# Kernel tuning notes

Measured on AMD Instinct MI355X. Metric: run time of the kernel, lower is better.

Reference implementation:

```python
import jax, jax.numpy as jnp
import numpy as np

N = 50000
T = 6
E = 800000
F_IN = 64
HID = 64
HEADS = 4
NEG_SLOPE = 0.2
BN_EPS = 1e-5


def _gat_layer(x, src, dst, W, att_src, att_dst, bias, concat):
    # x: [N, Fin]; W: [Fin, H*C]; att_*: [H, C]; src/dst: [E+N] (self loops appended)
    n = x.shape[0]
    H, C = att_src.shape
    xl = (x @ W).reshape(n, H, C)                     # [N, H, C]
    a_src = jnp.sum(xl * att_src[None], axis=-1)      # [N, H]
    a_dst = jnp.sum(xl * att_dst[None], axis=-1)      # [N, H]
    e = jax.nn.leaky_relu(a_src[src] + a_dst[dst], NEG_SLOPE)  # [E', H]
    # segment softmax over destination nodes (every node has a self loop)
    m = jax.ops.segment_max(e, dst, num_segments=n)
    ex = jnp.exp(e - m[dst])
    s = jax.ops.segment_sum(ex, dst, num_segments=n)
    alpha = ex / (s[dst] + 1e-16)                     # [E', H]
    msg = alpha[:, :, None] * xl[src]                 # [E', H, C]
    out = jax.ops.segment_sum(msg, dst, num_segments=n)  # [N, H, C]
    if concat:
        out = out.reshape(n, H * C)
    else:
        out = out.mean(axis=1)
    return out + bias


def _forward(x_seq, edge_index, W1, as1, ad1, b1, W2, as2, ad2, b2,
             cw1, cb1, g1, be1, cw2, cb2, g2, be2, lw1, lb1, lw2, lb2):
    n = x_seq.shape[1]
    self_loop = jnp.arange(n, dtype=edge_index.dtype)
    src = jnp.concatenate([edge_index[0], self_loop])
    dst = jnp.concatenate([edge_index[1], self_loop])

    def per_t(x):
        h = _gat_layer(x, src, dst, W1, as1, ad1, b1, concat=True)
        h = jax.nn.elu(h)
        h = _gat_layer(h, src, dst, W2, as2, ad2, b2, concat=False)
        h = jax.nn.elu(h)
        return h                                      # [N, HID]

    temporal = jax.vmap(per_t)(x_seq)                 # [T, N, HID]
    temporal = jnp.transpose(temporal, (1, 2, 0))     # [N, HID, T]

    def conv_bn_relu(t, cw, cb, g, be):
        y = jax.lax.conv_general_dilated(
            t, cw, window_strides=(1,), padding=[(1, 1)],
            dimension_numbers=('NCH', 'OIH', 'NCH')) + cb[None, :, None]
        # BatchNorm1d in eval mode, running_mean=0, running_var=1
        y = y * (g / jnp.sqrt(1.0 + BN_EPS))[None, :, None] + be[None, :, None]
        return jax.nn.relu(y)

    t = conv_bn_relu(temporal, cw1, cb1, g1, be1)
    t = conv_bn_relu(t, cw2, cb2, g2, be2)
    pooled = t.mean(axis=-1)                          # adaptive avg pool -> [N, HID]
    h = jax.nn.relu(pooled @ lw1 + lb1)
    logits = h @ lw2 + lb2                            # [N, 1]
    return logits


def setup_inputs() -> dict:
    key = jax.random.key(0)
    ks = jax.random.split(key, 20)
    C1 = HID // HEADS  # 16
    s = 0.1
    return {
        'x_seq': jax.random.normal(ks[0], (T, N, F_IN), jnp.float32),
        'edge_index': jax.random.randint(ks[1], (2, E), 0, N, jnp.int32),
        'W1': jax.random.normal(ks[2], (F_IN, HEADS * C1), jnp.float32) * s,
        'as1': jax.random.normal(ks[3], (HEADS, C1), jnp.float32) * s,
        'ad1': jax.random.normal(ks[4], (HEADS, C1), jnp.float32) * s,
        'b1': jnp.zeros((HEADS * C1,), jnp.float32),
        'W2': jax.random.normal(ks[5], (HID, HEADS * HID), jnp.float32) * s,
        'as2': jax.random.normal(ks[6], (HEADS, HID), jnp.float32) * s,
        'ad2': jax.random.normal(ks[7], (HEADS, HID), jnp.float32) * s,
        'b2': jnp.zeros((HID,), jnp.float32),
        'cw1': jax.random.normal(ks[8], (HID, HID, 3), jnp.float32) * s,
        'cb1': jnp.zeros((HID,), jnp.float32),
        'g1': jnp.ones((HID,), jnp.float32),
        'be1': jnp.zeros((HID,), jnp.float32),
        'cw2': jax.random.normal(ks[9], (HID, HID, 3), jnp.float32) * s,
        'cb2': jnp.zeros((HID,), jnp.float32),
        'g2': jnp.ones((HID,), jnp.float32),
        'be2': jnp.zeros((HID,), jnp.float32),
        'lw1': jax.random.normal(ks[10], (HID, HID // 2), jnp.float32) * s,
        'lb1': jnp.zeros((HID // 2,), jnp.float32),
        'lw2': jax.random.normal(ks[11], (HID // 2, 1), jnp.float32) * s,
        'lb2': jnp.zeros((1,), jnp.float32),
    }


def reference(x_seq, edge_index, W1, as1, ad1, b1, W2, as2, ad2, b2,
              cw1, cb1, g1, be1, cw2, cb2, g2, be2, lw1, lb1, lw2, lb2):
    return _forward(x_seq, edge_index, W1, as1, ad1, b1, W2, as2, ad2, b2,
                    cw1, cb1, g1, be1, cw2, cb2, g2, be2, lw1, lb1, lw2, lb2)
```

## Files before the change

kernel.cpp:

```cpp
#include <hip/hip_runtime.h>
#include <math.h>

#define NN 50000
#define EE 800000
#define TT 6

__device__ __forceinline__ float lrelu(float x){ return x > 0.f ? x : 0.2f*x; }
__device__ __forceinline__ float eluf(float x){ return x > 0.f ? x : expm1f(x); }

__global__ void k_init_counts(int* __restrict__ c){
  int i = blockIdx.x*256 + threadIdx.x;
  if (i < NN) c[i] = 1;
}

__global__ void k_hist(const int* __restrict__ dst, int* __restrict__ c){
  int i = blockIdx.x*256 + threadIdx.x;
  if (i < EE) atomicAdd(&c[dst[i]], 1);
}

__global__ void k_scanA(const int* __restrict__ cnt, int* __restrict__ excl,
                        int* __restrict__ bsum){
  __shared__ int sh[1024];
  int tid = threadIdx.x;
  int i = blockIdx.x*1024 + tid;
  int v = (i < NN) ? cnt[i] : 0;
  int x = v;
  sh[tid] = x; __syncthreads();
  for (int off = 1; off < 1024; off <<= 1){
    int y = (tid >= off) ? sh[tid - off] : 0;
    __syncthreads();
    x += y; sh[tid] = x; __syncthreads();
  }
  if (i < NN) excl[i] = x - v;
  if (tid == 1023) bsum[blockIdx.x] = x;
}

__global__ void k_scanB(int* __restrict__ bsum, int nb){
  if (threadIdx.x == 0){
    int run = 0;
    for (int b = 0; b < nb; ++b){ int t = bsum[b]; bsum[b] = run; run += t; }
  }
}

__global__ void k_scanC(const int* __restrict__ excl, const int* __restrict__ bsum,
                        int* __restrict__ rowptr, int* __restrict__ cursor){
  int i = blockIdx.x*1024 + threadIdx.x;
  if (i < NN){
    int v = excl[i] + bsum[blockIdx.x];
    rowptr[i] = v; cursor[i] = v;
  }
  if (i == 0) rowptr[NN] = EE + NN;
}

__global__ void k_scatter(const int* __restrict__ ei, int* __restrict__ cursor,
                          int* __restrict__ csr){
  int i = blockIdx.x*256 + threadIdx.x;
  if (i < EE){
    int d = ei[EE + i];
    int p = atomicAdd(&cursor[d], 1);
    csr[p] = ei[i];
  } else if (i < EE + NN){
    int v = i - EE;
    int p = atomicAdd(&cursor[v], 1);
    csr[p] = v;
  }
}

__global__ void k_prep(const float* __restrict__ W1, const float* __restrict__ as1,
                       const float* __restrict__ ad1,
                       const float* __restrict__ W2, const float* __restrict__ as2,
                       const float* __restrict__ ad2,
                       const float* __restrict__ cw1, const float* __restrict__ cw2,
                       const float* __restrict__ lw1,
                       float* __restrict__ Was1, float* __restrict__ Wad1,
                       float* __restrict__ Wat2, float* __restrict__ Wb,
                       float4* __restrict__ wq1, float4* __restrict__ wq2,
                       float* __restrict__ lw1t){
  int tid = threadIdx.x;
  int k = tid >> 2, h = tid & 3;
  float s1 = 0.f, d1 = 0.f, s2 = 0.f, d2 = 0.f;
  for (int c = 0; c < 16; ++c){
    float w = W1[k*64 + h*16 + c];
    s1 += w * as1[h*16 + c];
    d1 += w * ad1[h*16 + c];
  }
  for (int c = 0; c < 64; ++c){
    float w = W2[k*256 + h*64 + c];
    s2 += w * as2[h*64 + c];
    d2 += w * ad2[h*64 + c];
  }
  Was1[k*4+h] = s1; Wad1[k*4+h] = d1;
  Wat2[k*8 + h] = s2; Wat2[k*8 + 4 + h] = d2;
  for (int idx = tid; idx < 256*64; idx += 256){
    int kf = idx >> 6, c = idx & 63;
    int hh = kf >> 6, kk = kf & 63;
    Wb[idx] = W2[kk*256 + hh*64 + c];
  }
  for (int idx = tid; idx < 64*64; idx += 256){
    int o = idx >> 6, i = idx & 63;
    wq1[idx] = make_float4(cw1[o*192+i*3], cw1[o*192+i*3+1], cw1[o*192+i*3+2], 0.f);
    wq2[idx] = make_float4(cw2[o*192+i*3], cw2[o*192+i*3+1], cw2[o*192+i*3+2], 0.f);
  }
  for (int idx = tid; idx < 32*64; idx += 256){
    int j = idx >> 6, kk = idx & 63;
    lw1t[idx] = lw1[kk*32 + j];
  }
}

__global__ __launch_bounds__(256) void k_gemm_att1(const float* __restrict__ A,
                            const float* __restrict__ W,
                            const float* __restrict__ Was, const float* __restrict__ Wad,
                            float* __restrict__ Xl, float* __restrict__ a_src,
                            float* __restrict__ a_dst){
  __shared__ float At[64][16];
  int tid = threadIdx.x;
  int r0 = blockIdx.x * 16;
  {
    const float4* A4 = (const float4*)(A + (size_t)r0*64);
    float4 v = A4[tid];
    int r = tid >> 4, k4 = (tid & 15) << 2;
    At[k4+0][r] = v.x; At[k4+1][r] = v.y;
    At[k4+2][r] = v.z; At[k4+3][r] = v.w;
  }
  __syncthreads();
  int col = tid & 63;
  int rbase = (tid >> 6) << 2;
  float acc0=0.f, acc1=0.f, acc2=0.f, acc3=0.f;
  for (int k = 0; k < 64; ++k){
    float w = W[k*64 + col];
    float4 a4 = *(const float4*)&At[k][rbase];
    acc0 += a4.x*w; acc1 += a4.y*w; acc2 += a4.z*w; acc3 += a4.w*w;
  }
  Xl[(size_t)(r0+rbase+0)*64 + col] = acc0;
  Xl[(size_t)(r0+rbase+1)*64 + col] = acc1;
  Xl[(size_t)(r0+rbase+2)*64 + col] = acc2;
  Xl[(size_t)(r0+rbase+3)*64 + col] = acc3;
  if (tid < 128){
    int r = tid >> 3, jx = tid & 7;
    int h = jx & 3;
    const float* Wv = (jx < 4) ? Was : Wad;
    float a = 0.f;
    for (int k = 0; k < 64; ++k) a += At[k][r] * Wv[k*4 + h];
    if (jx < 4) a_src[(r0 + r)*4 + h] = a;
    else        a_dst[(r0 + r)*4 + h] = a;
  }
}

__global__ __launch_bounds__(256) void k_agg1(
                       const float* __restrict__ xl, const float* __restrict__ a_src,
                       const float* __restrict__ a_dst, const float* __restrict__ b1,
                       const float* __restrict__ Wat2,
                       const int* __restrict__ rowptr, const int* __restrict__ csr,
                       float* __restrict__ h1,
                       float* __restrict__ a_src2, float* __restrict__ a_dst2){
  int lane = threadIdx.x & 63;
  int wid  = threadIdx.x >> 6;
  int n = blockIdx.x*4 + wid;
  int h = lane >> 4;
  float ad = a_dst[n*4 + h];
  int rs = rowptr[n], re = rowptr[n+1];
  float s = 0.f, acc = 0.f;
  int j = rs;
  for (; j + 8 <= re; j += 8){
    int sn0=csr[j],   sn1=csr[j+1], sn2=csr[j+2], sn3=csr[j+3];
    int sn4=csr[j+4], sn5=csr[j+5], sn6=csr[j+6], sn7=csr[j+7];
    float e0=a_src[sn0*4+h], e1=a_src[sn1*4+h], e2=a_src[sn2*4+h], e3=a_src[sn3*4+h];
    float e4=a_src[sn4*4+h], e5=a_src[sn5*4+h], e6=a_src[sn6*4+h], e7=a_src[sn7*4+h];
    float x0=xl[(size_t)sn0*64+lane], x1=xl[(size_t)sn1*64+lane];
    float x2=xl[(size_t)sn2*64+lane], x3=xl[(size_t)sn3*64+lane];
    float x4=xl[(size_t)sn4*64+lane], x5=xl[(size_t)sn5*64+lane];
    float x6=xl[(size_t)sn6*64+lane], x7=xl[(size_t)sn7*64+lane];
    float p0=__expf(lrelu(e0+ad)), p1=__expf(lrelu(e1+ad));
    float p2=__expf(lrelu(e2+ad)), p3=__expf(lrelu(e3+ad));
    float p4=__expf(lrelu(e4+ad)), p5=__expf(lrelu(e5+ad));
    float p6=__expf(lrelu(e6+ad)), p7=__expf(lrelu(e7+ad));
    s += p0; acc += p0*x0;
    s += p1; acc += p1*x1;
    s += p2; acc += p2*x2;
    s += p3; acc += p3*x3;
    s += p4; acc += p4*x4;
    s += p5; acc += p5*x5;
    s += p6; acc += p6*x6;
    s += p7; acc += p7*x7;
  }
  for (; j < re; ++j){
    int sn = csr[j];
    float p = __expf(lrelu(a_src[sn*4+h] + ad));
    float x = xl[(size_t)sn*64 + lane];
    s += p; acc += p*x;
  }
  float hv = eluf(acc/(s + 1e-16f) + b1[lane]);
  h1[(size_t)n*64 + lane] = hv;
  float4 wA = ((const float4*)Wat2)[lane*2];
  float4 wB = ((const float4*)Wat2)[lane*2 + 1];
  float p[8];
  p[0]=hv*wA.x; p[1]=hv*wA.y; p[2]=hv*wA.z; p[3]=hv*wA.w;
  p[4]=hv*wB.x; p[5]=hv*wB.y; p[6]=hv*wB.z; p[7]=hv*wB.w;
#pragma unroll
  for (int off = 32; off >= 1; off >>= 1){
#pragma unroll
    for (int q = 0; q < 8; ++q) p[q] += __shfl_xor(p[q], off);
  }
  if (lane == 0){
    ((float4*)a_src2)[n] = make_float4(p[0],p[1],p[2],p[3]);
    ((float4*)a_dst2)[n] = make_float4(p[4],p[5],p[6],p[7]);
  }
}

__global__ __launch_bounds__(256) void k_agg2(
                       const float* __restrict__ h1, const float* __restrict__ a_src,
                       const float* __restrict__ a_dst,
                       const int* __restrict__ rowptr, const int* __restrict__ csr,
                       float* __restrict__ agg){
  int lane = threadIdx.x & 63;
  int wid  = threadIdx.x >> 6;
  int n = blockIdx.x*4 + wid;
  float4 ad = ((const float4*)a_dst)[n];
  int rs = rowptr[n], re = rowptr[n+1];
  float s0=0.f,s1=0.f,s2=0.f,s3=0.f;
  float g0=0.f,g1=0.f,g2=0.f,g3=0.f;
  int j = rs;
  for (; j + 8 <= re; j += 8){
    int sa=csr[j],   sb=csr[j+1], sc=csr[j+2], sd=csr[j+3];
    int se=csr[j+4], sf=csr[j+5], sg=csr[j+6], sh=csr[j+7];
    float4 ea = ((const float4*)a_src)[sa];
    float4 eb = ((const float4*)a_src)[sb];
    float4 ec = ((const float4*)a_src)[sc];
    float4 ed = ((const float4*)a_src)[sd];
    float4 ee = ((const float4*)a_src)[se];
    float4 ef = ((const float4*)a_src)[sf];
    float4 eg = ((const float4*)a_src)[sg];
    float4 eh = ((const float4*)a_src)[sh];
    float xa = h1[(size_t)sa*64 + lane];
    float xb = h1[(size_t)sb*64 + lane];
    float xc = h1[(size_t)sc*64 + lane];
    float xd = h1[(size_t)sd*64 + lane];
    float xe = h1[(size_t)se*64 + lane];
    float xf = h1[(size_t)sf*64 + lane];
    float xg = h1[(size_t)sg*64 + lane];
    float xh = h1[(size_t)sh*64 + lane];
    float pa0=__expf(lrelu(ea.x+ad.x)), pa1=__expf(lrelu(ea.y+ad.y));
    float pa2=__expf(lrelu(ea.z+ad.z)), pa3=__expf(lrelu(ea.w+ad.w));
    float pb0=__expf(lrelu(eb.x+ad.x)), pb1=__expf(lrelu(eb.y+ad.y));
    float pb2=__expf(lrelu(eb.z+ad.z)), pb3=__expf(lrelu(eb.w+ad.w));
    float pc0=__expf(lrelu(ec.x+ad.x)), pc1=__expf(lrelu(ec.y+ad.y));
    float pc2=__expf(lrelu(ec.z+ad.z)), pc3=__expf(lrelu(ec.w+ad.w));
    float pd0=__expf(lrelu(ed.x+ad.x)), pd1=__expf(lrelu(ed.y+ad.y));
    float pd2=__expf(lrelu(ed.z+ad.z)), pd3=__expf(lrelu(ed.w+ad.w));
    float pe0=__expf(lrelu(ee.x+ad.x)), pe1=__expf(lrelu(ee.y+ad.y));
    float pe2=__expf(lrelu(ee.z+ad.z)), pe3=__expf(lrelu(ee.w+ad.w));
    float pf0=__expf(lrelu(ef.x+ad.x)), pf1=__expf(lrelu(ef.y+ad.y));
    float pf2=__expf(lrelu(ef.z+ad.z)), pf3=__expf(lrelu(ef.w+ad.w));
    float pg0=__expf(lrelu(eg.x+ad.x)), pg1=__expf(lrelu(eg.y+ad.y));
    float pg2=__expf(lrelu(eg.z+ad.z)), pg3=__expf(lrelu(eg.w+ad.w));
    float ph0=__expf(lrelu(eh.x+ad.x)), ph1=__expf(lrelu(eh.y+ad.y));
    float ph2=__expf(lrelu(eh.z+ad.z)), ph3=__expf(lrelu(eh.w+ad.w));
    s0 += pa0+pb0+pc0+pd0+pe0+pf0+pg0+ph0;
    g0 += pa0*xa + pb0*xb + pc0*xc + pd0*xd + pe0*xe + pf0*xf + pg0*xg + ph0*xh;
    s1 += pa1+pb1+pc1+pd1+pe1+pf1+pg1+ph1;
    g1 += pa1*xa + pb1*xb + pc1*xc + pd1*xd + pe1*xe + pf1*xf + pg1*xg + ph1*xh;
    s2 += pa2+pb2+pc2+pd2+pe2+pf2+pg2+ph2;
    g2 += pa2*xa + pb2*xb + pc2*xc + pd2*xd + pe2*xe + pf2*xf + pg2*xg + ph2*xh;
    s3 += pa3+pb3+pc3+pd3+pe3+pf3+pg3+ph3;
    g3 += pa3*xa + pb3*xb + pc3*xc + pd3*xd + pe3*xe + pf3*xf + pg3*xg + ph3*xh;
  }
  for (; j < re; ++j){
    int sn = csr[j];
    float4 ev = ((const float4*)a_src)[sn];
    float x = h1[(size_t)sn*64 + lane];
    float p0=__expf(lrelu(ev.x+ad.x)), p1=__expf(lrelu(ev.y+ad.y));
    float p2=__expf(lrelu(ev.z+ad.z)), p3=__expf(lrelu(ev.w+ad.w));
    s0 += p0; g0 += p0*x;
    s1 += p1; g1 += p1*x;
    s2 += p2; g2 += p2*x;
    s3 += p3; g3 += p3*x;
  }
  size_t base = (size_t)n*256 + lane;
  agg[base      ] = g0/(s0 + 1e-16f);
  agg[base +  64] = g1/(s1 + 1e-16f);
  agg[base + 128] = g2/(s2 + 1e-16f);
  agg[base + 192] = g3/(s3 + 1e-16f);
}

__global__ __launch_bounds__(256) void k_out2(const float* __restrict__ agg,
                                              const float* __restrict__ Wb,
                                              const float* __restrict__ b2,
                                              float* __restrict__ ht){
  __shared__ float AtF[256*20];
  int tid = threadIdx.x;
  int r0 = blockIdx.x * 16;
  const float4* A4 = (const float4*)(agg + (size_t)r0*256);
#pragma unroll
  for (int jj = 0; jj < 4; ++jj){
    int m = tid + 256*jj;
    float4 v = A4[m];
    int row = m >> 6, k0 = (m & 63) << 2;
    AtF[(k0+0)*20 + row] = v.x;
    AtF[(k0+1)*20 + row] = v.y;
    AtF[(k0+2)*20 + row] = v.z;
    AtF[(k0+3)*20 + row] = v.w;
  }
  __syncthreads();
  int col = tid & 63;
  int rbase = (tid >> 6) << 2;
  float acc0=0.f, acc1=0.f, acc2=0.f, acc3=0.f;
  for (int k = 0; k < 256; ++k){
    float w = Wb[(size_t)k*64 + col];
    float4 a4 = *(const float4*)&AtF[k*20 + rbase];
    acc0 += a4.x*w; acc1 += a4.y*w; acc2 += a4.z*w; acc3 += a4.w*w;
  }
  float bb = b2[col];
  ht[(size_t)(r0+rbase+0)*64 + col] = eluf(0.25f*acc0 + bb);
  ht[(size_t)(r0+rbase+1)*64 + col] = eluf(0.25f*acc1 + bb);
  ht[(size_t)(r0+rbase+2)*64 + col] = eluf(0.25f*acc2 + bb);
  ht[(size_t)(r0+rbase+3)*64 + col] = eluf(0.25f*acc3 + bb);
}

__global__ __launch_bounds__(256) void k_conv(const float* __restrict__ htb,
    const float4* __restrict__ wq1, const float* __restrict__ cb1,
    const float* __restrict__ g1,   const float* __restrict__ be1,
    const float4* __restrict__ wq2, const float* __restrict__ cb2,
    const float* __restrict__ g2,   const float* __restrict__ be2,
    float* __restrict__ pooledG){
  __shared__ float X[64*198];
  int tid  = threadIdx.x;
  int lane = tid & 63;
  int w    = __builtin_amdgcn_readfirstlane(tid >> 6);
  int nn   = lane & 31;
  int half = lane >> 5;
  int n0 = blockIdx.x*32;
  int n  = n0 + nn;
  int ob = w*16 + half*8;

#pragma unroll
  for (int k = 0; k < 8; ++k){
    int p  = k*256 + tid;
    int ch = p & 63, ns = p >> 6;
    int nsrc = n0 + ns; if (nsrc >= NN) nsrc = NN-1;
    float xv[6];
#pragma unroll
    for (int t = 0; t < 6; ++t) xv[t] = htb[((size_t)t*NN + nsrc)*64 + ch];
#pragma unroll
    for (int t = 0; t < 6; ++t) X[ch*198 + t*33 + ns] = xv[t];
  }
  __syncthreads();

  float acc[8][6];
#pragma unroll
  for (int o = 0; o < 8; ++o){
    float c = cb1[ob+o];
#pragma unroll
    for (int t = 0; t < 6; ++t) acc[o][t] = c;
  }
  for (int i = 0; i < 64; ++i){
    const float* xp = X + i*198 + nn;
    float x1 = xp[0], x2 = xp[33], x3 = xp[66];
    float x4 = xp[99], x5 = xp[132], x6 = xp[165];
#pragma unroll
    for (int o = 0; o < 8; ++o){
      float4 wv = wq1[(ob+o)*64 + i];
      acc[o][0] += wv.y*x1 + wv.z*x2;
      acc[o][1] += wv.x*x1 + wv.y*x2 + wv.z*x3;
      acc[o][2] += wv.x*x2 + wv.y*x3 + wv.z*x4;
      acc[o][3] += wv.x*x3 + wv.y*x4 + wv.z*x5;
      acc[o][4] += wv.x*x4 + wv.y*x5 + wv.z*x6;
      acc[o][5] += wv.x*x5 + wv.y*x6;
    }
  }
  __syncthreads();
#pragma unroll
  for (int o = 0; o < 8; ++o){
    float bns = g1[ob+o]*rsqrtf(1.f + 1e-5f), be = be1[ob+o];
    float* xp = X + (ob+o)*198 + nn;
#pragma unroll
    for (int t = 0; t < 6; ++t) xp[t*33] = fmaxf(acc[o][t]*bns + be, 0.f);
  }
  __syncthreads();

#pragma unroll
  for (int o = 0; o < 8; ++o){
    float c = cb2[ob+o];
#pragma unroll
    for (int t = 0; t < 6; ++t) acc[o][t] = c;
  }
  for (int i = 0; i < 64; ++i){
    const float* xp = X + i*198 + nn;
    float x1 = xp[0], x2 = xp[33], x3 = xp[66];
    float x4 = xp[99], x5 = xp[132], x6 = xp[165];
#pragma unroll
    for (int o = 0; o < 8; ++o){
      float4 wv = wq2[(ob+o)*64 + i];
      acc[o][0] += wv.y*x1 + wv.z*x2;
      acc[o][1] += wv.x*x1 + wv.y*x2 + wv.z*x3;
      acc[o][2] += wv.x*x2 + wv.y*x3 + wv.z*x4;
      acc[o][3] += wv.x*x3 + wv.y*x4 + wv.z*x5;
      acc[o][4] += wv.x*x4 + wv.y*x5 + wv.z*x6;
      acc[o][5] += wv.x*x5 + wv.y*x6;
    }
  }
  if (n < NN){
#pragma unroll
    for (int o = 0; o < 8; ++o){
      float bns = g2[ob+o]*rsqrtf(1.f + 1e-5f), be = be2[ob+o];
      float pooled = 0.f;
#pragma unroll
      for (int t = 0; t < 6; ++t) pooled += fmaxf(acc[o][t]*bns + be, 0.f);
      pooledG[(size_t)(ob+o)*NN + n] = pooled*(1.f/6.f);
    }
  }
}

__global__ __launch_bounds__(256) void k_mlp(const float* __restrict__ pooledG,
    const float* __restrict__ lw1t, const float* __restrict__ lb1,
    const float* __restrict__ lw2,  const float* __restrict__ lb2,
    float* __restrict__ out){
  int lane = threadIdx.x & 63;
  int w = __builtin_amdgcn_readfirstlane(threadIdx.x >> 6);
  int n = (blockIdx.x*4 + w)*64 + lane;
  int nc = (n < NN) ? n : (NN-1);
  float p[64];
#pragma unroll 16
  for (int o = 0; o < 64; ++o) p[o] = pooledG[(size_t)o*NN + nc];
  float po = 0.f;
  for (int j = 0; j < 32; ++j){
    float hj = lb1[j];
#pragma unroll 16
    for (int k = 0; k < 64; ++k) hj += p[k] * lw1t[j*64 + k];
    po += fmaxf(hj, 0.f) * lw2[j];
  }
  if (n < NN) out[n] = po + lb2[0];
}

extern "C" void kernel_launch(void* const* d_in, const int* in_sizes, int n_in,
                              void* d_out, int out_size, void* d_ws, size_t ws_size,
                              hipStream_t stream) {
  const float* x_seq = (const float*)d_in[0];
  const int*   ei    = (const int*)  d_in[1];
  const float* W1  = (const float*)d_in[2];
  const float* as1 = (const float*)d_in[3];
  const float* ad1 = (const float*)d_in[4];
  const float* b1  = (const float*)d_in[5];
  const float* W2  = (const float*)d_in[6];
  const float* as2 = (const float*)d_in[7];
  const float* ad2 = (const float*)d_in[8];
  const float* b2  = (const float*)d_in[9];
  const float* cw1 = (const float*)d_in[10];
  const float* cb1 = (const float*)d_in[11];
  const float* g1  = (const float*)d_in[12];
  const float* be1 = (const float*)d_in[13];
  const float* cw2 = (const float*)d_in[14];
  const float* cb2 = (const float*)d_in[15];
  const float* g2  = (const float*)d_in[16];
  const float* be2 = (const float*)d_in[17];
  const float* lw1 = (const float*)d_in[18];
  const float* lb1 = (const float*)d_in[19];
  const float* lw2 = (const float*)d_in[20];
  const float* lb2 = (const float*)d_in[21];
  float* out = (float*)d_out;

  char* wp = (char*)d_ws;
  auto alloc = [&](size_t bytes) -> char* {
    char* p = wp; wp += (bytes + 255) & ~(size_t)255; return p;
  };
  int*   counts = (int*)  alloc(NN*sizeof(int));
  int*   excl   = (int*)  alloc(NN*sizeof(int));
  int*   bsum   = (int*)  alloc(64*sizeof(int));
  int*   rowptr = (int*)  alloc((NN+1)*sizeof(int));
  int*   cursor = (int*)  alloc(NN*sizeof(int));
  int*   csr    = (int*)  alloc((size_t)(EE+NN)*sizeof(int));
  float* a_src1 = (float*)alloc((size_t)NN*4*sizeof(float));
  float* a_dst1 = (float*)alloc((size_t)NN*4*sizeof(float));
  float* a_src2 = (float*)alloc((size_t)NN*4*sizeof(float));
  float* a_dst2 = (float*)alloc((size_t)NN*4*sizeof(float));
  float* h1     = (float*)alloc((size_t)NN*64*sizeof(float));
  float* agg    = (float*)alloc((size_t)NN*256*sizeof(float));
  float* xl1    = agg;
  float* htb    = (float*)alloc((size_t)TT*NN*64*sizeof(float));
  float* pooledG= (float*)alloc((size_t)64*NN*sizeof(float));
  float* Was1 = (float*)alloc(256*sizeof(float));
  float* Wad1 = (float*)alloc(256*sizeof(float));
  float* Wat2 = (float*)alloc(64*8*sizeof(float));
  float* Wb   = (float*)alloc(256*64*sizeof(float));
  float4* wq1 = (float4*)alloc(64*64*sizeof(float4));
  float4* wq2 = (float4*)alloc(64*64*sizeof(float4));
  float* lw1t = (float*)alloc(32*64*sizeof(float));

  const int NBSCAN = (NN + 1023)/1024;
  k_init_counts<<<(NN+255)/256, 256, 0, stream>>>(counts);
  k_hist<<<(EE+255)/256, 256, 0, stream>>>(ei + EE, counts);
  k_scanA<<<NBSCAN, 1024, 0, stream>>>(counts, excl, bsum);
  k_scanB<<<1, 64, 0, stream>>>(bsum, NBSCAN);
  k_scanC<<<NBSCAN, 1024, 0, stream>>>(excl, bsum, rowptr, cursor);
  k_scatter<<<(EE+NN+255)/256, 256, 0, stream>>>(ei, cursor, csr);
  k_prep<<<1, 256, 0, stream>>>(W1, as1, ad1, W2, as2, ad2, cw1, cw2, lw1,
                                Was1, Wad1, Wat2, Wb, wq1, wq2, lw1t);

  for (int t = 0; t < TT; ++t){
    const float* xt = x_seq + (size_t)t*NN*64;
    k_gemm_att1<<<NN/16, 256, 0, stream>>>(xt, W1, Was1, Wad1, xl1, a_src1, a_dst1);
    k_agg1<<<NN/4, 256, 0, stream>>>(xl1, a_src1, a_dst1, b1, Wat2, rowptr, csr,
                                     h1, a_src2, a_dst2);
    k_agg2<<<NN/4, 256, 0, stream>>>(h1, a_src2, a_dst2, rowptr, csr, agg);
    k_out2<<<NN/16, 256, 0, stream>>>(agg, Wb, b2, htb + (size_t)t*NN*64);
  }
  k_conv<<<(NN+31)/32, 256, 0, stream>>>(htb, wq1, cb1, g1, be1, wq2, cb2, g2, be2,
                                         pooledG);
  k_mlp<<<(NN+255)/256, 256, 0, stream>>>(pooledG, lw1t, lb1, lw2, lb2, out);
}
```

Measured before the change: 1.554 ms.

## Retile out2 GEMM and conv kernel, shrink gather unroll in aggregation

The edge-gather loops in both aggregation kernels are unrolled by 4 instead of 8, which lowers register pressure and may raise occupancy at the cost of fewer loads in flight. The layer-2 output GEMM is re-tiled so each block stages 64 rows of agg in padded shared memory. Each lane owns one row and accumulates 16 output columns with wave-uniform weight reads, and results are written back through shared memory for coalesced stores. The temporal conv kernel now processes 16 nodes per block with 4 output channels per thread, giving smaller shared memory and register footprints and more blocks.

```diff
diff --git a/kernel.cpp b/kernel.cpp
--- a/kernel.cpp
+++ b/kernel.cpp
@@ -161,27 +161,17 @@
   int rs = rowptr[n], re = rowptr[n+1];
   float s = 0.f, acc = 0.f;
   int j = rs;
-  for (; j + 8 <= re; j += 8){
-    int sn0=csr[j],   sn1=csr[j+1], sn2=csr[j+2], sn3=csr[j+3];
-    int sn4=csr[j+4], sn5=csr[j+5], sn6=csr[j+6], sn7=csr[j+7];
+  for (; j + 4 <= re; j += 4){
+    int sn0=csr[j], sn1=csr[j+1], sn2=csr[j+2], sn3=csr[j+3];
     float e0=a_src[sn0*4+h], e1=a_src[sn1*4+h], e2=a_src[sn2*4+h], e3=a_src[sn3*4+h];
-    float e4=a_src[sn4*4+h], e5=a_src[sn5*4+h], e6=a_src[sn6*4+h], e7=a_src[sn7*4+h];
     float x0=xl[(size_t)sn0*64+lane], x1=xl[(size_t)sn1*64+lane];
     float x2=xl[(size_t)sn2*64+lane], x3=xl[(size_t)sn3*64+lane];
-    float x4=xl[(size_t)sn4*64+lane], x5=xl[(size_t)sn5*64+lane];
-    float x6=xl[(size_t)sn6*64+lane], x7=xl[(size_t)sn7*64+lane];
     float p0=__expf(lrelu(e0+ad)), p1=__expf(lrelu(e1+ad));
     float p2=__expf(lrelu(e2+ad)), p3=__expf(lrelu(e3+ad));
-    float p4=__expf(lrelu(e4+ad)), p5=__expf(lrelu(e5+ad));
-    float p6=__expf(lrelu(e6+ad)), p7=__expf(lrelu(e7+ad));
     s += p0; acc += p0*x0;
     s += p1; acc += p1*x1;
     s += p2; acc += p2*x2;
     s += p3; acc += p3*x3;
-    s += p4; acc += p4*x4;
-    s += p5; acc += p5*x5;
-    s += p6; acc += p6*x6;
-    s += p7; acc += p7*x7;
   }
   for (; j < re; ++j){
     int sn = csr[j];
@@ -220,25 +210,16 @@
   float s0=0.f,s1=0.f,s2=0.f,s3=0.f;
   float g0=0.f,g1=0.f,g2=0.f,g3=0.f;
   int j = rs;
-  for (; j + 8 <= re; j += 8){
-    int sa=csr[j],   sb=csr[j+1], sc=csr[j+2], sd=csr[j+3];
-    int se=csr[j+4], sf=csr[j+5], sg=csr[j+6], sh=csr[j+7];
+  for (; j + 4 <= re; j += 4){
+    int sa=csr[j], sb=csr[j+1], sc=csr[j+2], sd=csr[j+3];
     float4 ea = ((const float4*)a_src)[sa];
     float4 eb = ((const float4*)a_src)[sb];
     float4 ec = ((const float4*)a_src)[sc];
     float4 ed = ((const float4*)a_src)[sd];
-    float4 ee = ((const float4*)a_src)[se];
-    float4 ef = ((const float4*)a_src)[sf];
-    float4 eg = ((const float4*)a_src)[sg];
-    float4 eh = ((const float4*)a_src)[sh];
     float xa = h1[(size_t)sa*64 + lane];
     float xb = h1[(size_t)sb*64 + lane];
     float xc = h1[(size_t)sc*64 + lane];
     float xd = h1[(size_t)sd*64 + lane];
-    float xe = h1[(size_t)se*64 + lane];
-    float xf = h1[(size_t)sf*64 + lane];
-    float xg = h1[(size_t)sg*64 + lane];
-    float xh = h1[(size_t)sh*64 + lane];
     float pa0=__expf(lrelu(ea.x+ad.x)), pa1=__expf(lrelu(ea.y+ad.y));
     float pa2=__expf(lrelu(ea.z+ad.z)), pa3=__expf(lrelu(ea.w+ad.w));
     float pb0=__expf(lrelu(eb.x+ad.x)), pb1=__expf(lrelu(eb.y+ad.y));
@@ -247,22 +228,10 @@
     float pc2=__expf(lrelu(ec.z+ad.z)), pc3=__expf(lrelu(ec.w+ad.w));
     float pd0=__expf(lrelu(ed.x+ad.x)), pd1=__expf(lrelu(ed.y+ad.y));
     float pd2=__expf(lrelu(ed.z+ad.z)), pd3=__expf(lrelu(ed.w+ad.w));
-    float pe0=__expf(lrelu(ee.x+ad.x)), pe1=__expf(lrelu(ee.y+ad.y));
-    float pe2=__expf(lrelu(ee.z+ad.z)), pe3=__expf(lrelu(ee.w+ad.w));
-    float pf0=__expf(lrelu(ef.x+ad.x)), pf1=__expf(lrelu(ef.y+ad.y));
-    float pf2=__expf(lrelu(ef.z+ad.z)), pf3=__expf(lrelu(ef.w+ad.w));
-    float pg0=__expf(lrelu(eg.x+ad.x)), pg1=__expf(lrelu(eg.y+ad.y));
-    float pg2=__expf(lrelu(eg.z+ad.z)), pg3=__expf(lrelu(eg.w+ad.w));
-    float ph0=__expf(lrelu(eh.x+ad.x)), ph1=__expf(lrelu(eh.y+ad.y));
-    float ph2=__expf(lrelu(eh.z+ad.z)), ph3=__expf(lrelu(eh.w+ad.w));
-    s0 += pa0+pb0+pc0+pd0+pe0+pf0+pg0+ph0;
-    g0 += pa0*xa + pb0*xb + pc0*xc + pd0*xd + pe0*xe + pf0*xf + pg0*xg + ph0*xh;
-    s1 += pa1+pb1+pc1+pd1+pe1+pf1+pg1+ph1;
-    g1 += pa1*xa + pb1*xb + pc1*xc + pd1*xd + pe1*xe + pf1*xf + pg1*xg + ph1*xh;
-    s2 += pa2+pb2+pc2+pd2+pe2+pf2+pg2+ph2;
-    g2 += pa2*xa + pb2*xb + pc2*xc + pd2*xd + pe2*xe + pf2*xf + pg2*xg + ph2*xh;
-    s3 += pa3+pb3+pc3+pd3+pe3+pf3+pg3+ph3;
-    g3 += pa3*xa + pb3*xb + pc3*xc + pd3*xd + pe3*xe + pf3*xf + pg3*xg + ph3*xh;
+    s0 += pa0+pb0+pc0+pd0; g0 += pa0*xa + pb0*xb + pc0*xc + pd0*xd;
+    s1 += pa1+pb1+pc1+pd1; g1 += pa1*xa + pb1*xb + pc1*xc + pd1*xd;
+    s2 += pa2+pb2+pc2+pd2; g2 += pa2*xa + pb2*xb + pc2*xc + pd2*xd;
+    s3 += pa3+pb3+pc3+pd3; g3 += pa3*xa + pb3*xb + pc3*xc + pd3*xd;
   }
   for (; j < re; ++j){
     int sn = csr[j];
@@ -286,34 +255,42 @@
                                               const float* __restrict__ Wb,
                                               const float* __restrict__ b2,
                                               float* __restrict__ ht){
-  __shared__ float AtF[256*20];
+  __shared__ float A[64*257];
   int tid = threadIdx.x;
-  int r0 = blockIdx.x * 16;
-  const float4* A4 = (const float4*)(agg + (size_t)r0*256);
-#pragma unroll
-  for (int jj = 0; jj < 4; ++jj){
-    int m = tid + 256*jj;
-    float4 v = A4[m];
-    int row = m >> 6, k0 = (m & 63) << 2;
-    AtF[(k0+0)*20 + row] = v.x;
-    AtF[(k0+1)*20 + row] = v.y;
-    AtF[(k0+2)*20 + row] = v.z;
-    AtF[(k0+3)*20 + row] = v.w;
-  }
-  __syncthreads();
-  int col = tid & 63;
-  int rbase = (tid >> 6) << 2;
-  float acc0=0.f, acc1=0.f, acc2=0.f, acc3=0.f;
+  int lane = tid & 63;
+  int w = __builtin_amdgcn_readfirstlane(tid >> 6);
+  int r0 = blockIdx.x * 64;
+  for (int jj = 0; jj < 64; ++jj){
+    int m = jj*256 + tid;
+    int row = m >> 8, k = m & 255;
+    int rsrc = r0 + row; if (rsrc >= NN) rsrc = NN-1;
+    A[row*257 + k] = agg[(size_t)rsrc*256 + k];
+  }
+  __syncthreads();
+  const float* __restrict__ Wbw = Wb + w*16;
+  float acc[16];
+#pragma unroll
+  for (int jq = 0; jq < 16; ++jq) acc[jq] = 0.f;
+  const float* Ar = A + lane*257;
+#pragma unroll 8
   for (int k = 0; k < 256; ++k){
-    float w = Wb[(size_t)k*64 + col];
-    float4 a4 = *(const float4*)&AtF[k*20 + rbase];
-    acc0 += a4.x*w; acc1 += a4.y*w; acc2 += a4.z*w; acc3 += a4.w*w;
-  }
-  float bb = b2[col];
-  ht[(size_t)(r0+rbase+0)*64 + col] = eluf(0.25f*acc0 + bb);
-  ht[(size_t)(r0+rbase+1)*64 + col] = eluf(0.25f*acc1 + bb);
-  ht[(size_t)(r0+rbase+2)*64 + col] = eluf(0.25f*acc2 + bb);
-  ht[(size_t)(r0+rbase+3)*64 + col] = eluf(0.25f*acc3 + bb);
+    float a = Ar[k];
+#pragma unroll
+    for (int jq = 0; jq < 16; ++jq) acc[jq] += a * Wbw[(k<<6) + jq];
+  }
+  __syncthreads();
+#pragma unroll
+  for (int jq = 0; jq < 16; ++jq){
+    int c = w*16 + jq;
+    A[lane*65 + c] = eluf(0.25f*acc[jq] + b2[c]);
+  }
+  __syncthreads();
+  for (int jj = 0; jj < 16; ++jj){
+    int m = jj*256 + tid;
+    int row = m >> 6, c = m & 63;
+    int rdst = r0 + row;
+    if (rdst < NN) ht[(size_t)rdst*64 + c] = A[row*65 + c];
+  }
 }
 
 __global__ __launch_bounds__(256) void k_conv(const float* __restrict__ htb,
@@ -322,91 +299,88 @@
     const float4* __restrict__ wq2, const float* __restrict__ cb2,
     const float* __restrict__ g2,   const float* __restrict__ be2,
     float* __restrict__ pooledG){
-  __shared__ float X[64*198];
+  __shared__ float X[64*103];
   int tid  = threadIdx.x;
   int lane = tid & 63;
   int w    = __builtin_amdgcn_readfirstlane(tid >> 6);
-  int nn   = lane & 31;
-  int half = lane >> 5;
-  int n0 = blockIdx.x*32;
+  int nn   = lane & 15;
+  int oq   = lane >> 4;
+  int n0 = blockIdx.x*16;
   int n  = n0 + nn;
-  int ob = w*16 + half*8;
-
-#pragma unroll
-  for (int k = 0; k < 8; ++k){
+  int ob = w*16 + oq*4;
+
+#pragma unroll
+  for (int k = 0; k < 4; ++k){
     int p  = k*256 + tid;
     int ch = p & 63, ns = p >> 6;
-    int nsrc = n0 + ns; if (nsrc >= NN) nsrc = NN-1;
     float xv[6];
 #pragma unroll
-    for (int t = 0; t < 6; ++t) xv[t] = htb[((size_t)t*NN + nsrc)*64 + ch];
-#pragma unroll
-    for (int t = 0; t < 6; ++t) X[ch*198 + t*33 + ns] = xv[t];
-  }
-  __syncthreads();
-
-  float acc[8][6];
-#pragma unroll
-  for (int o = 0; o < 8; ++o){
-    float c = cb1[ob+o];
-#pragma unroll
-    for (int t = 0; t < 6; ++t) acc[o][t] = c;
+    for (int t = 0; t < 6; ++t) xv[t] = htb[((size_t)t*NN + n0 + ns)*64 + ch];
+#pragma unroll
+    for (int t = 0; t < 6; ++t) X[ch*103 + t*17 + ns] = xv[t];
+  }
+  __syncthreads();
+
+  float acc[4][6];
+#pragma unroll
+  for (int q = 0; q < 4; ++q){
+    float c = cb1[ob+q];
+#pragma unroll
+    for (int t = 0; t < 6; ++t) acc[q][t] = c;
   }
   for (int i = 0; i < 64; ++i){
-    const float* xp = X + i*198 + nn;
-    float x1 = xp[0], x2 = xp[33], x3 = xp[66];
-    float x4 = xp[99], x5 = xp[132], x6 = xp[165];
-#pragma unroll
-    for (int o = 0; o < 8; ++o){
-      float4 wv = wq1[(ob+o)*64 + i];
-      acc[o][0] += wv.y*x1 + wv.z*x2;
-      acc[o][1] += wv.x*x1 + wv.y*x2 + wv.z*x3;
-      acc[o][2] += wv.x*x2 + wv.y*x3 + wv.z*x4;
-      acc[o][3] += wv.x*x3 + wv.y*x4 + wv.z*x5;
-      acc[o][4] += wv.x*x4 + wv.y*x5 + wv.z*x6;
-      acc[o][5] += wv.x*x5 + wv.y*x6;
+    const float* xp = X + i*103 + nn;
+    float x1 = xp[0], x2 = xp[17], x3 = xp[34];
+    float x4 = xp[51], x5 = xp[68], x6 = xp[85];
+#pragma unroll
+    for (int q = 0; q < 4; ++q){
+      float4 wv = wq1[(ob+q)*64 + i];
+      acc[q][0] += wv.y*x1 + wv.z*x2;
+      acc[q][1] += wv.x*x1 + wv.y*x2 + wv.z*x3;
+      acc[q][2] += wv.x*x2 + wv.y*x3 + wv.z*x4;
+      acc[q][3] += wv.x*x3 + wv.y*x4 + wv.z*x5;
+      acc[q][4] += wv.x*x4 + wv.y*x5 + wv.z*x6;
+      acc[q][5] += wv.x*x5 + wv.y*x6;
     }
   }
   __syncthreads();
 #pragma unroll
-  for (int o = 0; o < 8; ++o){
-    float bns = g1[ob+o]*rsqrtf(1.f + 1e-5f), be = be1[ob+o];
-    float* xp = X + (ob+o)*198 + nn;
-#pragma unroll
-    for (int t = 0; t < 6; ++t) xp[t*33] = fmaxf(acc[o][t]*bns + be, 0.f);
-  }
-  __syncthreads();
-
-#pragma unroll
-  for (int o = 0; o < 8; ++o){
-    float c = cb2[ob+o];
-#pragma unroll
-    for (int t = 0; t < 6; ++t) acc[o][t] = c;
+  for (int q = 0; q < 4; ++q){
+    float bns = g1[ob+q]*rsqrtf(1.f + 1e-5f), be = be1[ob+q];
+    float* xp = X + (ob+q)*103 + nn;
+#pragma unroll
+    for (int t = 0; t < 6; ++t) xp[t*17] = fmaxf(acc[q][t]*bns + be, 0.f);
+  }
+  __syncthreads();
+
+#pragma unroll
+  for (int q = 0; q < 4; ++q){
+    float c = cb2[ob+q];
+#pragma unroll
+    for (int t = 0; t < 6; ++t) acc[q][t] = c;
   }
   for (int i = 0; i < 64; ++i){
-    const float* xp = X + i*198 + nn;
-    float x1 = xp[0], x2 = xp[33], x3 = xp[66];
-    float x4 = xp[99], x5 = xp[132], x6 = xp[165];
-#pragma unroll
-    for (int o = 0; o < 8; ++o){
-      float4 wv = wq2[(ob+o)*64 + i];
-      acc[o][0] += wv.y*x1 + wv.z*x2;
-      acc[o][1] += wv.x*x1 + wv.y*x2 + wv.z*x3;
-      acc[o][2] += wv.x*x2 + wv.y*x3 + wv.z*x4;
-      acc[o][3] += wv.x*x3 + wv.y*x4 + wv.z*x5;
-      acc[o][4] += wv.x*x4 + wv.y*x5 + wv.z*x6;
-      acc[o][5] += wv.x*x5 + wv.y*x6;
+    const float* xp = X + i*103 + nn;
+    float x1 = xp[0], x2 = xp[17], x3 = xp[34];
+    float x4 = xp[51], x5 = xp[68], x6 = xp[85];
+#pragma unroll
+    for (int q = 0; q < 4; ++q){
+      float4 wv = wq2[(ob+q)*64 + i];
+      acc[q][0] += wv.y*x1 + wv.z*x2;
+      acc[q][1] += wv.x*x1 + wv.y*x2 + wv.z*x3;
+      acc[q][2] += wv.x*x2 + wv.y*x3 + wv.z*x4;
+      acc[q][3] += wv.x*x3 + wv.y*x4 + wv.z*x5;
+      acc[q][4] += wv.x*x4 + wv.y*x5 + wv.z*x6;
+      acc[q][5] += wv.x*x5 + wv.y*x6;
     }
   }
-  if (n < NN){
-#pragma unroll
-    for (int o = 0; o < 8; ++o){
-      float bns = g2[ob+o]*rsqrtf(1.f + 1e-5f), be = be2[ob+o];
-      float pooled = 0.f;
-#pragma unroll
-      for (int t = 0; t < 6; ++t) pooled += fmaxf(acc[o][t]*bns + be, 0.f);
-      pooledG[(size_t)(ob+o)*NN + n] = pooled*(1.f/6.f);
-    }
+#pragma unroll
+  for (int q = 0; q < 4; ++q){
+    float bns = g2[ob+q]*rsqrtf(1.f + 1e-5f), be = be2[ob+q];
+    float pooled = 0.f;
+#pragma unroll
+    for (int t = 0; t < 6; ++t) pooled += fmaxf(acc[q][t]*bns + be, 0.f);
+    pooledG[(size_t)(ob+q)*NN + n] = pooled*(1.f/6.f);
   }
 }
 
@@ -495,15 +469,16 @@
   k_prep<<<1, 256, 0, stream>>>(W1, as1, ad1, W2, as2, ad2, cw1, cw2, lw1,
                                 Was1, Wad1, Wat2, Wb, wq1, wq2, lw1t);
 
+  const int NOUT2 = (NN + 63)/64;
   for (int t = 0; t < TT; ++t){
     const float* xt = x_seq + (size_t)t*NN*64;
     k_gemm_att1<<<NN/16, 256, 0, stream>>>(xt, W1, Was1, Wad1, xl1, a_src1, a_dst1);
     k_agg1<<<NN/4, 256, 0, stream>>>(xl1, a_src1, a_dst1, b1, Wat2, rowptr, csr,
                                      h1, a_src2, a_dst2);
     k_agg2<<<NN/4, 256, 0, stream>>>(h1, a_src2, a_dst2, rowptr, csr, agg);
-    k_out2<<<NN/16, 256, 0, stream>>>(agg, Wb, b2, htb + (size_t)t*NN*64);
-  }
-  k_conv<<<(NN+31)/32, 256, 0, stream>>>(htb, wq1, cb1, g1, be1, wq2, cb2, g2, be2,
-                                         pooledG);
+    k_out2<<<NOUT2, 256, 0, stream>>>(agg, Wb, b2, htb + (size_t)t*NN*64);
+  }
+  k_conv<<<NN/16, 256, 0, stream>>>(htb, wq1, cb1, g1, be1, wq2, cb2, g2, be2,
+                                    pooledG);
   k_mlp<<<(NN+255)/256, 256, 0, stream>>>(pooledG, lw1t, lb1, lw2, lb2, out);
 }
```

New measurement: 1.475 ms. 1.05x faster.
